# Performance work log

Measured on AMD Instinct MI355X. Metric: run time of the kernel, lower is better.

## Reference

```python
import jax, jax.numpy as jnp
import numpy as np

ALPHA = 16
M_FACTORS = [8, 16, 8]
N_FACTORS = [8, 16, 8]


def setup_inputs() -> dict:
    key = jax.random.key(0)
    ks = jax.random.split(key, 9)
    B, S, D = 8, 2048, 1024
    r = 8
    x = jax.random.normal(ks[0], (B, S, D), dtype=jnp.float32)
    W = jax.random.normal(ks[1], (D, D), dtype=jnp.float32) * 0.02
    b = jax.random.normal(ks[2], (D,), dtype=jnp.float32) * 0.02
    # m-cores: (r_prev, m_i, r_next), first rank = 1
    core0 = jax.random.normal(ks[3], (1, 8, r), dtype=jnp.float32) * 0.1
    core1 = jax.random.normal(ks[4], (r, 16, r), dtype=jnp.float32) * 0.1
    core2 = jax.random.normal(ks[5], (r, 8, r), dtype=jnp.float32) * 0.1
    # n-cores: (r_prev, n_i, r_next), last rank = 1
    core3 = jax.random.normal(ks[6], (r, 8, r), dtype=jnp.float32) * 0.1
    core4 = jax.random.normal(ks[7], (r, 16, r), dtype=jnp.float32) * 0.1
    core5 = jax.random.normal(ks[8], (r, 8, 1), dtype=jnp.float32) * 0.1
    return {"x": x, "W": W, "b": b, "core0": core0, "core1": core1,
            "core2": core2, "core3": core3, "core4": core4, "core5": core5}


def tensorized_multiplication(x, m_cores, n_cores, m_factors):
    B, S, _ = x.shape
    # [B, 1, S, m_k, ..., m_1] : input dim split into m_factors, reversed
    tt = x.reshape((B, S) + tuple(m_factors[::-1]))[:, None]
    for core in m_cores:
        # contract trailing m-factor and current rank, new rank at axis 1
        tt = jnp.einsum('br...m,rmp->bp...', tt, core)
    for core in n_cores:
        # expand n-factor at the end, carry rank at axis 1
        tt = jnp.einsum('br...,rnp->bp...n', tt, core)
    # tt: [B, 1, S, n_1, ..., n_k] -> [B, S, prod(n_factors)]
    return tt.reshape(B, S, -1)


def reference(x, W, b, core0, core1, core2, core3, core4, core5):
    z = tensorized_multiplication(x, [core0, core1, core2],
                                  [core3, core4, core5], M_FACTORS)
    base = jnp.einsum('bsd,od->bso', x, W) + b  # nn.Linear: x @ W.T + b
    return base + z * ALPHA
```

## Files before the change

### kernel.cpp

```cpp
#include <hip/hip_runtime.h>
#include <hip/hip_bf16.h>


#define D_DIM 1024
#define BS_ROWS 16384
#define ALPHA_F 16.0f
#define BM 128
#define BN 128

using bf16   = __bf16;
using bf16x8 = __attribute__((ext_vector_type(8))) __bf16;
using bf16x4 = __attribute__((ext_vector_type(4))) __bf16;
using f32x4  = __attribute__((ext_vector_type(4))) float;

#define GPTR(p) (const __attribute__((address_space(1))) void*)(p)
#define SPTR(p) (__attribute__((address_space(3))) void*)(p)

__global__ __launch_bounds__(256) void make_mn_kernel(
    const float* __restrict__ c0, const float* __restrict__ c1,
    const float* __restrict__ c2, const float* __restrict__ c3,
    const float* __restrict__ c4, const float* __restrict__ c5,
    float* __restrict__ Mws, float* __restrict__ NTws)
{
    __shared__ float sh[128 * 9];
    const int tid = threadIdx.x;

    if (blockIdx.x < 32) {
        for (int e = tid; e < 1024; e += 256) {
            int p2 = e & 7, i2i1 = e >> 3;
            int i1 = i2i1 & 7, i2 = i2i1 >> 3;
            float s = 0.f;
            for (int p1 = 0; p1 < 8; ++p1)
                s += c0[i1 * 8 + p1] * c1[p1 * 128 + i2 * 8 + p2];
            sh[i2i1 * 9 + p2] = s;
        }
        __syncthreads();
        int e = blockIdx.x * 256 + tid;
        int p3 = e & 7, d = e >> 3;
        int i1 = d & 7, i2 = (d >> 3) & 15, i3 = d >> 7;
        float s = 0.f;
        for (int p2 = 0; p2 < 8; ++p2)
            s += sh[(i2 * 8 + i1) * 9 + p2] * c2[p2 * 64 + i3 * 8 + p3];
        Mws[e] = s;
    } else {
        for (int e = tid; e < 1024; e += 256) {
            int p4 = e & 7, nn = e >> 3;
            int n2 = nn >> 3, n3 = nn & 7;
            float s = 0.f;
            for (int p5 = 0; p5 < 8; ++p5)
                s += c4[p4 * 128 + n2 * 8 + p5] * c5[p5 * 8 + n3];
            sh[nn * 9 + p4] = s;
        }
        __syncthreads();
        int e = (blockIdx.x - 32) * 256 + tid;
        int r3 = e & 7, o = e >> 3;
        int n1 = o >> 7, nn = o & 127;
        float s = 0.f;
        for (int p4 = 0; p4 < 8; ++p4)
            s += c3[r3 * 64 + n1 * 8 + p4] * sh[nn * 9 + p4];
        NTws[o * 8 + r3] = s;
    }
}

__global__ __launch_bounds__(256) void weff_cast_kernel(
    const float* __restrict__ X, const float* __restrict__ W,
    const float* __restrict__ Mws, const float* __restrict__ NTws,
    bf16* __restrict__ Weff, bf16* __restrict__ Xb)
{
    const int tid = threadIdx.x;
    if (blockIdx.x >= 512) {
        size_t i = ((size_t)(blockIdx.x - 512) * 256 + tid) * 8;
        f32x4 a = *(const f32x4*)&X[i];
        f32x4 b = *(const f32x4*)&X[i + 4];
        bf16x8 v;
        v[0] = (bf16)a[0]; v[1] = (bf16)a[1]; v[2] = (bf16)a[2]; v[3] = (bf16)a[3];
        v[4] = (bf16)b[0]; v[5] = (bf16)b[1]; v[6] = (bf16)b[2]; v[7] = (bf16)b[3];
        *(bf16x8*)&Xb[i] = v;
        return;
    }
    int e  = blockIdx.x * 256 + tid;
    int o  = e >> 7;
    int d0 = (e & 127) * 8;
    f32x4 nt0 = *(const f32x4*)&NTws[o * 8];
    f32x4 nt1 = *(const f32x4*)&NTws[o * 8 + 4];
    f32x4 w0 = *(const f32x4*)&W[(size_t)o * D_DIM + d0];
    f32x4 w1 = *(const f32x4*)&W[(size_t)o * D_DIM + d0 + 4];
    bf16x8 res;
    for (int k = 0; k < 8; ++k) {
        f32x4 m0 = *(const f32x4*)&Mws[(d0 + k) * 8];
        f32x4 m1 = *(const f32x4*)&Mws[(d0 + k) * 8 + 4];
        float acc = m0[0]*nt0[0] + m0[1]*nt0[1] + m0[2]*nt0[2] + m0[3]*nt0[3]
                  + m1[0]*nt1[0] + m1[1]*nt1[1] + m1[2]*nt1[2] + m1[3]*nt1[3];
        float w = (k < 4) ? w0[k] : w1[k - 4];
        res[k] = (bf16)(w + ALPHA_F * acc);
    }
    *(bf16x8*)&Weff[(size_t)o * D_DIM + d0] = res;
}

#define TBM 256
#define TBN 256
#define TBK 64
#define ABYT (TBM * TBK * 2)
#define BBYT (TBN * TBK * 2)
#define BUF5 (ABYT + BBYT)
#define NT5  (D_DIM / TBK)

__global__ __launch_bounds__(512, 2) void gemm_pipe5_kernel(
    const bf16* __restrict__ Xb,
    const bf16* __restrict__ Weff,
    const float* __restrict__ bias,
    float* __restrict__ Out)
{
    extern __shared__ __attribute__((aligned(16))) char smem[];

    const int tid  = threadIdx.x;
    const int wave = tid >> 6, lane = tid & 63;

    const int bid   = blockIdx.x;
    const int slot  = (bid & 7) * 32 + (bid >> 3);
    const int mtile = slot >> 2;
    const int ntile = slot & 3;

    const int wr = wave >> 2, wc = wave & 3;
    const int l15 = lane & 15, quad = lane >> 4;
    const int rsw = l15 & 7;

    const int srow   = wave * 32 + (lane >> 3);
    const int gchunk = (lane & 7) ^ (lane >> 3);
    const bf16* asrc = Xb   + (size_t)(mtile * TBM + srow) * D_DIM + gchunk * 8;
    const bf16* bsrc = Weff + (size_t)(ntile * TBN + srow) * D_DIM + gchunk * 8;
    const int woff = wave * 4096;

    auto STAGE = [&](int bo, int t) {
        const bf16* ap = asrc + t * TBK;
        const bf16* bp = bsrc + t * TBK;
#pragma unroll
        for (int j = 0; j < 4; ++j)
            __builtin_amdgcn_global_load_lds(GPTR(ap + (size_t)j * 8 * D_DIM),
                                             SPTR(smem + bo + woff + j * 1024), 16, 0, 0);
#pragma unroll
        for (int j = 0; j < 4; ++j)
            __builtin_amdgcn_global_load_lds(GPTR(bp + (size_t)j * 8 * D_DIM),
                                             SPTR(smem + bo + ABYT + woff + j * 1024), 16, 0, 0);
    };

    f32x4 acc[8][4];
#pragma unroll
    for (int i = 0; i < 8; ++i)
#pragma unroll
        for (int j = 0; j < 4; ++j)
#pragma unroll
            for (int r = 0; r < 4; ++r) acc[i][j][r] = 0.f;

    auto COMPUTE = [&](int bo) {
        const char* Ab = smem + bo;
        const char* Bb = smem + bo + ABYT;
#pragma unroll
        for (int kk = 0; kk < 2; ++kk) {
            const int sb = ((kk * 4 + quad) ^ rsw) * 16;
            bf16x8 bfr[4];
#pragma unroll
            for (int j = 0; j < 4; ++j)
                bfr[j] = *(const bf16x8*)(Bb + (wc * 64 + j * 16 + l15) * 128 + sb);
#pragma unroll
            for (int i = 0; i < 8; ++i) {
                bf16x8 af = *(const bf16x8*)(Ab + (wr * 128 + i * 16 + l15) * 128 + sb);
                __builtin_amdgcn_s_setprio(1);
#pragma unroll
                for (int j = 0; j < 4; ++j)
                    acc[i][j] = __builtin_amdgcn_mfma_f32_16x16x32_bf16(
                        af, bfr[j], acc[i][j], 0, 0, 0);
                __builtin_amdgcn_s_setprio(0);
            }
        }
    };

    STAGE(0, 0);
    asm volatile("s_waitcnt vmcnt(0)" ::: "memory");
    __builtin_amdgcn_s_barrier();
    __builtin_amdgcn_sched_barrier(0);

    int cur = 0;
    for (int t = 0; t < NT5 - 1; ++t) {
        STAGE((cur ^ 1) * BUF5, t + 1);
        COMPUTE(cur * BUF5);
        asm volatile("s_waitcnt vmcnt(0) lgkmcnt(0)" ::: "memory");
        __builtin_amdgcn_s_barrier();
        __builtin_amdgcn_sched_barrier(0);
        cur ^= 1;
    }
    COMPUTE(cur * BUF5);

    float bj[4];
#pragma unroll
    for (int j = 0; j < 4; ++j)
        bj[j] = bias[ntile * TBN + wc * 64 + j * 16 + l15];
#pragma unroll
    for (int i = 0; i < 8; ++i) {
        int row0 = mtile * TBM + wr * 128 + i * 16 + quad * 4;
#pragma unroll
        for (int r = 0; r < 4; ++r) {
            float* orow = Out + (size_t)(row0 + r) * D_DIM + ntile * TBN + wc * 64 + l15;
#pragma unroll
            for (int j = 0; j < 4; ++j)
                orow[j * 16] = acc[i][j][r] + bj[j];
        }
    }
}

__global__ __launch_bounds__(256) void gemm_bb_kernel(
    const bf16* __restrict__ Xb,
    const bf16* __restrict__ Weff,
    const float* __restrict__ bias,
    float* __restrict__ Out)
{
    __shared__ __align__(16) bf16 As[BM][64];
    __shared__ __align__(16) bf16 Bs[BN][64];

    const int tid  = threadIdx.x;
    const int wave = tid >> 6, lane = tid & 63;
    const int mtile = blockIdx.x, ntile = blockIdx.y;
    const int wr = wave >> 1, wc = wave & 1;
    const int l15 = lane & 15, quad = lane >> 4;

    const int srow = wave * 32 + (lane >> 3);
    const int gchunk = (lane & 7) ^ (lane >> 3);
    const bf16* asrc = Xb   + (size_t)(mtile * BM + srow) * D_DIM + gchunk * 8;
    const bf16* bsrc = Weff + (size_t)(ntile * BN + srow) * D_DIM + gchunk * 8;
    char* abase = (char*)&As[0][0] + wave * 4096;
    char* bbase = (char*)&Bs[0][0] + wave * 4096;

    const int rsw = l15 & 7;

    f32x4 acc[4][4];
    for (int i = 0; i < 4; ++i)
        for (int j = 0; j < 4; ++j)
            for (int r = 0; r < 4; ++r) acc[i][j][r] = 0.f;

    for (int kt = 0; kt < D_DIM / 64; ++kt) {
        const int ko = kt * 64;
        for (int j = 0; j < 4; ++j) {
            __builtin_amdgcn_global_load_lds(GPTR(asrc + (size_t)j * 8 * D_DIM + ko),
                                             SPTR(abase + j * 1024), 16, 0, 0);
            __builtin_amdgcn_global_load_lds(GPTR(bsrc + (size_t)j * 8 * D_DIM + ko),
                                             SPTR(bbase + j * 1024), 16, 0, 0);
        }
        __syncthreads();
        for (int kk = 0; kk < 2; ++kk) {
            const int lc = kk * 4 + quad;
            const int sc = (lc ^ rsw) * 8;
            bf16x8 af[4], bfr[4];
            for (int i = 0; i < 4; ++i)
                af[i] = *(const bf16x8*)&As[wr * 64 + i * 16 + l15][sc];
            for (int j = 0; j < 4; ++j)
                bfr[j] = *(const bf16x8*)&Bs[wc * 64 + j * 16 + l15][sc];
            for (int i = 0; i < 4; ++i)
                for (int j = 0; j < 4; ++j)
                    acc[i][j] = __builtin_amdgcn_mfma_f32_16x16x32_bf16(
                        af[i], bfr[j], acc[i][j], 0, 0, 0);
        }
        __syncthreads();
    }

    float bj[4];
    for (int j = 0; j < 4; ++j)
        bj[j] = bias[ntile * BN + wc * 64 + j * 16 + l15];
    for (int i = 0; i < 4; ++i) {
        int row0 = mtile * BM + wr * 64 + i * 16 + quad * 4;
        for (int r = 0; r < 4; ++r) {
            float* orow = Out + (size_t)(row0 + r) * D_DIM + ntile * BN + wc * 64 + l15;
            for (int j = 0; j < 4; ++j)
                orow[j * 16] = acc[i][j][r] + bj[j];
        }
    }
}

__global__ __launch_bounds__(256) void gemm_bias_kernel(
    const float* __restrict__ X,
    const bf16* __restrict__ Weff,
    const float* __restrict__ bias,
    float* __restrict__ Out)
{
    __shared__ __align__(16) bf16 As[BM][32];
    __shared__ __align__(16) bf16 Bs[BN][32];

    const int tid  = threadIdx.x;
    const int wave = tid >> 6, lane = tid & 63;
    const int mtile = blockIdx.x, ntile = blockIdx.y;
    const int wr = wave >> 1, wc = wave & 1;
    const int l15 = lane & 15, quad = lane >> 4;

    const int ar = tid >> 1, ah = tid & 1;
    const float* xsrc = X + (size_t)(mtile * BM + ar) * D_DIM + ah * 16;
    bf16* adst = &As[ar][ah * 16];

    const bf16* bsrc0 = Weff + (size_t)(ntile * BN + wave * 32 + (lane >> 2)) * D_DIM
                        + (lane & 3) * 8;
    const bf16* bsrc1 = bsrc0 + 16 * D_DIM;
    char* bbase = (char*)&Bs[0][0];
    void* bdst0 = bbase + wave * 2048;
    void* bdst1 = bbase + wave * 2048 + 1024;

    f32x4 acc[4][4];
    for (int i = 0; i < 4; ++i)
        for (int j = 0; j < 4; ++j)
            for (int r = 0; r < 4; ++r) acc[i][j][r] = 0.f;

    for (int kt = 0; kt < D_DIM / 32; ++kt) {
        __builtin_amdgcn_global_load_lds(GPTR(bsrc0 + kt * 32), SPTR(bdst0), 16, 0, 0);
        __builtin_amdgcn_global_load_lds(GPTR(bsrc1 + kt * 32), SPTR(bdst1), 16, 0, 0);

        const f32x4* xp = (const f32x4*)(xsrc + kt * 32);
        f32x4 f0 = xp[0], f1 = xp[1], f2 = xp[2], f3 = xp[3];
        bf16x8 p0, p1;
        p0[0] = (bf16)f0[0]; p0[1] = (bf16)f0[1]; p0[2] = (bf16)f0[2]; p0[3] = (bf16)f0[3];
        p0[4] = (bf16)f1[0]; p0[5] = (bf16)f1[1]; p0[6] = (bf16)f1[2]; p0[7] = (bf16)f1[3];
        p1[0] = (bf16)f2[0]; p1[1] = (bf16)f2[1]; p1[2] = (bf16)f2[2]; p1[3] = (bf16)f2[3];
        p1[4] = (bf16)f3[0]; p1[5] = (bf16)f3[1]; p1[6] = (bf16)f3[2]; p1[7] = (bf16)f3[3];
        *(bf16x8*)adst = p0;
        *(bf16x8*)(adst + 8) = p1;

        __syncthreads();

        bf16x8 af[4], bfr[4];
        for (int i = 0; i < 4; ++i)
            af[i] = *(const bf16x8*)&As[wr * 64 + i * 16 + l15][quad * 8];
        for (int j = 0; j < 4; ++j)
            bfr[j] = *(const bf16x8*)&Bs[wc * 64 + j * 16 + l15][quad * 8];
        for (int i = 0; i < 4; ++i)
            for (int j = 0; j < 4; ++j)
                acc[i][j] = __builtin_amdgcn_mfma_f32_16x16x32_bf16(
                    af[i], bfr[j], acc[i][j], 0, 0, 0);

        __syncthreads();
    }

    float bj[4];
    for (int j = 0; j < 4; ++j)
        bj[j] = bias[ntile * BN + wc * 64 + j * 16 + l15];
    for (int i = 0; i < 4; ++i) {
        int row0 = mtile * BM + wr * 64 + i * 16 + quad * 4;
        for (int r = 0; r < 4; ++r) {
            float* orow = Out + (size_t)(row0 + r) * D_DIM + ntile * BN + wc * 64 + l15;
            for (int j = 0; j < 4; ++j)
                orow[j * 16] = acc[i][j][r] + bj[j];
        }
    }
}

__global__ __launch_bounds__(256) void build_weff_fused_kernel(
    const float* __restrict__ W,
    const float* __restrict__ c0, const float* __restrict__ c1,
    const float* __restrict__ c2, const float* __restrict__ c3,
    const float* __restrict__ c4, const float* __restrict__ c5,
    bf16* __restrict__ Weff)
{
    __shared__ float t2[1024];
    __shared__ float Msh[8192];
    const int tid = threadIdx.x;
    const int o = blockIdx.x;

    for (int e = tid; e < 1024; e += 256) {
        int p2 = e & 7, i2i1 = e >> 3;
        int i1 = i2i1 & 7, i2 = i2i1 >> 3;
        float s = 0.f;
        for (int p1 = 0; p1 < 8; ++p1)
            s += c0[i1 * 8 + p1] * c1[p1 * 128 + i2 * 8 + p2];
        t2[e] = s;
    }
    __syncthreads();
    for (int e = tid; e < 8192; e += 256) {
        int p3 = e & 7, d = e >> 3;
        int i1 = d & 7, i2 = (d >> 3) & 15, i3 = d >> 7;
        float s = 0.f;
        for (int p2 = 0; p2 < 8; ++p2)
            s += t2[(i2 * 8 + i1) * 8 + p2] * c2[p2 * 64 + i3 * 8 + p3];
        Msh[e] = s;
    }
    int n1 = o >> 7, nn = o & 127, n2 = nn >> 3, n3 = nn & 7;
    float v[8];
    for (int p4 = 0; p4 < 8; ++p4) {
        float s = 0.f;
        for (int p5 = 0; p5 < 8; ++p5)
            s += c4[p4 * 128 + n2 * 8 + p5] * c5[p5 * 8 + n3];
        v[p4] = s;
    }
    float ncol[8];
    for (int r3 = 0; r3 < 8; ++r3) {
        float s = 0.f;
        for (int p4 = 0; p4 < 8; ++p4)
            s += c3[r3 * 64 + n1 * 8 + p4] * v[p4];
        ncol[r3] = s;
    }
    __syncthreads();

    int d0 = tid * 4;
    f32x4 w = *(const f32x4*)&W[o * D_DIM + d0];
    bf16x4 res;
    for (int k = 0; k < 4; ++k) {
        float acc = 0.f;
        for (int r = 0; r < 8; ++r)
            acc += Msh[(d0 + k) * 8 + r] * ncol[r];
        res[k] = (bf16)(w[k] + ALPHA_F * acc);
    }
    *(bf16x4*)&Weff[o * D_DIM + d0] = res;
}

extern "C" void kernel_launch(void* const* d_in, const int* in_sizes, int n_in,
                              void* d_out, int out_size, void* d_ws, size_t ws_size,
                              hipStream_t stream) {
    const float* x  = (const float*)d_in[0];
    const float* W  = (const float*)d_in[1];
    const float* b  = (const float*)d_in[2];
    const float* c0 = (const float*)d_in[3];
    const float* c1 = (const float*)d_in[4];
    const float* c2 = (const float*)d_in[5];
    const float* c3 = (const float*)d_in[6];
    const float* c4 = (const float*)d_in[7];
    const float* c5 = (const float*)d_in[8];
    float* out = (float*)d_out;

    char* ws = (char*)d_ws;
    bf16*  Weff = (bf16*)ws;
    float* Mws  = (float*)(ws + 2u * 1024u * 1024u);
    float* NTws = Mws + 8192;
    bf16*  Xb   = (bf16*)(ws + 4u * 1024u * 1024u);
    const size_t need = 4u * 1024u * 1024u + (size_t)BS_ROWS * D_DIM * 2u;

    static int smem_ok = -1;
    if (smem_ok < 0) {
        hipError_t e = hipFuncSetAttribute((const void*)gemm_pipe5_kernel,
                                           hipFuncAttributeMaxDynamicSharedMemorySize,
                                           2 * BUF5);
        smem_ok = (e == hipSuccess) ? 1 : 0;
    }

    if (ws_size >= need) {
        make_mn_kernel<<<64, 256, 0, stream>>>(c0, c1, c2, c3, c4, c5, Mws, NTws);
        weff_cast_kernel<<<512 + 8192, 256, 0, stream>>>(x, W, Mws, NTws, Weff, Xb);
        if (smem_ok) {
            gemm_pipe5_kernel<<<dim3(256), 512, 2 * BUF5, stream>>>(Xb, Weff, b, out);
        } else {
            dim3 grid(BS_ROWS / BM, D_DIM / BN);
            gemm_bb_kernel<<<grid, 256, 0, stream>>>(Xb, Weff, b, out);
        }
    } else {
        build_weff_fused_kernel<<<D_DIM, 256, 0, stream>>>(W, c0, c1, c2, c3, c4, c5, Weff);
        dim3 grid(BS_ROWS / BM, D_DIM / BN);
        gemm_bias_kernel<<<grid, 256, 0, stream>>>(x, Weff, b, out);
    }
}
```

Measured before the change: 164.9 us.

## Interleave next-tile loads with MFMA phases in a ping-pong GEMM schedule

Rewrites the GEMM main loop so each K-step runs in four phases. The global-to-LDS loads for the next tile are issued in units between the early phases, and LDS reads of A fragments are split per phase, with barriers that keep waves in lockstep. The aim is to overlap memory traffic with MFMA work more finely and reduce LDS-read stalls ahead of the matrix ops. The extra barriers per phase add synchronisation overhead, and the staging layout changes to 128-row units.

```diff
diff --git a/kernel.cpp b/kernel.cpp
--- a/kernel.cpp
+++ b/kernel.cpp
@@ -100,12 +100,11 @@
 #define TBM 256
 #define TBN 256
 #define TBK 64
-#define ABYT (TBM * TBK * 2)
-#define BBYT (TBN * TBK * 2)
-#define BUF5 (ABYT + BBYT)
-#define NT5  (D_DIM / TBK)
-
-__global__ __launch_bounds__(512, 2) void gemm_pipe5_kernel(
+#define ABYT 32768
+#define BUF6 65536
+#define NT6  (D_DIM / TBK)
+
+__global__ __launch_bounds__(512, 2) void gemm_pipe6_kernel(
     const bf16* __restrict__ Xb,
     const bf16* __restrict__ Weff,
     const float* __restrict__ bias,
@@ -125,71 +124,89 @@
     const int l15 = lane & 15, quad = lane >> 4;
     const int rsw = l15 & 7;
 
-    const int srow   = wave * 32 + (lane >> 3);
+    const int urow   = wave * 8 + (lane >> 3);
     const int gchunk = (lane & 7) ^ (lane >> 3);
-    const bf16* asrc = Xb   + (size_t)(mtile * TBM + srow) * D_DIM + gchunk * 8;
-    const bf16* bsrc = Weff + (size_t)(ntile * TBN + srow) * D_DIM + gchunk * 8;
-    const int woff = wave * 4096;
-
-    auto STAGE = [&](int bo, int t) {
-        const bf16* ap = asrc + t * TBK;
-        const bf16* bp = bsrc + t * TBK;
+    const bf16* aB = Xb   + (size_t)(mtile * TBM) * D_DIM + gchunk * 8;
+    const bf16* bB = Weff + (size_t)(ntile * TBN) * D_DIM + gchunk * 8;
+    const int lco = wave * 1024 + lane * 16;
+
+    auto STAGE_UNIT = [&](int bo, int t, int u) {
+        const bf16* src = (u < 2)
+            ? aB + (size_t)(u * 128 + urow) * D_DIM + t * TBK
+            : bB + (size_t)((u - 2) * 128 + urow) * D_DIM + t * TBK;
+        char* dst = smem + bo + (u < 2 ? 0 : ABYT) + (u & 1) * 16384 + lco;
+#pragma unroll
+        for (int j = 0; j < 2; ++j)
+            __builtin_amdgcn_global_load_lds(GPTR(src + (size_t)j * 64 * D_DIM),
+                                             SPTR(dst + j * 8192), 16, 0, 0);
+    };
+
+    f32x4 acc[8][4];
+#pragma unroll
+    for (int i = 0; i < 8; ++i)
 #pragma unroll
         for (int j = 0; j < 4; ++j)
-            __builtin_amdgcn_global_load_lds(GPTR(ap + (size_t)j * 8 * D_DIM),
-                                             SPTR(smem + bo + woff + j * 1024), 16, 0, 0);
-#pragma unroll
-        for (int j = 0; j < 4; ++j)
-            __builtin_amdgcn_global_load_lds(GPTR(bp + (size_t)j * 8 * D_DIM),
-                                             SPTR(smem + bo + ABYT + woff + j * 1024), 16, 0, 0);
-    };
-
-    f32x4 acc[8][4];
-#pragma unroll
-    for (int i = 0; i < 8; ++i)
-#pragma unroll
-        for (int j = 0; j < 4; ++j)
 #pragma unroll
             for (int r = 0; r < 4; ++r) acc[i][j][r] = 0.f;
 
-    auto COMPUTE = [&](int bo) {
-        const char* Ab = smem + bo;
-        const char* Bb = smem + bo + ABYT;
-#pragma unroll
-        for (int kk = 0; kk < 2; ++kk) {
-            const int sb = ((kk * 4 + quad) ^ rsw) * 16;
-            bf16x8 bfr[4];
-#pragma unroll
-            for (int j = 0; j < 4; ++j)
-                bfr[j] = *(const bf16x8*)(Bb + (wc * 64 + j * 16 + l15) * 128 + sb);
-#pragma unroll
-            for (int i = 0; i < 8; ++i) {
-                bf16x8 af = *(const bf16x8*)(Ab + (wr * 128 + i * 16 + l15) * 128 + sb);
-                __builtin_amdgcn_s_setprio(1);
-#pragma unroll
-                for (int j = 0; j < 4; ++j)
-                    acc[i][j] = __builtin_amdgcn_mfma_f32_16x16x32_bf16(
-                        af, bfr[j], acc[i][j], 0, 0, 0);
-                __builtin_amdgcn_s_setprio(0);
-            }
-        }
-    };
-
-    STAGE(0, 0);
+    STAGE_UNIT(0, 0, 2); STAGE_UNIT(0, 0, 3);
+    STAGE_UNIT(0, 0, 0); STAGE_UNIT(0, 0, 1);
     asm volatile("s_waitcnt vmcnt(0)" ::: "memory");
     __builtin_amdgcn_s_barrier();
     __builtin_amdgcn_sched_barrier(0);
 
-    int cur = 0;
-    for (int t = 0; t < NT5 - 1; ++t) {
-        STAGE((cur ^ 1) * BUF5, t + 1);
-        COMPUTE(cur * BUF5);
-        asm volatile("s_waitcnt vmcnt(0) lgkmcnt(0)" ::: "memory");
-        __builtin_amdgcn_s_barrier();
-        __builtin_amdgcn_sched_barrier(0);
-        cur ^= 1;
-    }
-    COMPUTE(cur * BUF5);
+    for (int t = 0; t < NT6; ++t) {
+        const int bo = (t & 1) * BUF6;
+        const int bn = ((t + 1) & 1) * BUF6;
+        const bool more = (t + 1 < NT6);
+        const char* Ab = smem + bo;
+        const char* Bb = smem + bo + ABYT;
+
+        bf16x8 bfr[4][2];
+#pragma unroll
+        for (int p = 0; p < 4; ++p) {
+            if (p == 0 && more) { STAGE_UNIT(bn, t + 1, 2); STAGE_UNIT(bn, t + 1, 3); }
+            if (p == 1 && more) { STAGE_UNIT(bn, t + 1, 0); STAGE_UNIT(bn, t + 1, 1); }
+
+            if (p == 0) {
+#pragma unroll
+                for (int j = 0; j < 4; ++j)
+#pragma unroll
+                    for (int kk = 0; kk < 2; ++kk)
+                        bfr[j][kk] = *(const bf16x8*)(Bb
+                            + (wc * 64 + j * 16 + l15) * 128
+                            + ((kk * 4 + quad) ^ rsw) * 16);
+            }
+            bf16x8 af[2][2];
+#pragma unroll
+            for (int ii = 0; ii < 2; ++ii)
+#pragma unroll
+                for (int kk = 0; kk < 2; ++kk)
+                    af[ii][kk] = *(const bf16x8*)(Ab
+                        + (wr * 128 + (2 * p + ii) * 16 + l15) * 128
+                        + ((kk * 4 + quad) ^ rsw) * 16);
+
+            __builtin_amdgcn_s_barrier();
+            asm volatile("s_waitcnt lgkmcnt(0)" ::: "memory");
+            __builtin_amdgcn_s_setprio(1);
+#pragma unroll
+            for (int kk = 0; kk < 2; ++kk)
+#pragma unroll
+                for (int ii = 0; ii < 2; ++ii)
+#pragma unroll
+                    for (int j = 0; j < 4; ++j)
+                        acc[2 * p + ii][j] = __builtin_amdgcn_mfma_f32_16x16x32_bf16(
+                            af[ii][kk], bfr[j][kk], acc[2 * p + ii][j], 0, 0, 0);
+            __builtin_amdgcn_s_setprio(0);
+            if (p < 3) __builtin_amdgcn_s_barrier();
+        }
+
+        if (more) {
+            asm volatile("s_waitcnt vmcnt(0)" ::: "memory");
+            __builtin_amdgcn_s_barrier();
+            __builtin_amdgcn_sched_barrier(0);
+        }
+    }
 
     float bj[4];
 #pragma unroll
@@ -429,9 +446,9 @@
 
     static int smem_ok = -1;
     if (smem_ok < 0) {
-        hipError_t e = hipFuncSetAttribute((const void*)gemm_pipe5_kernel,
+        hipError_t e = hipFuncSetAttribute((const void*)gemm_pipe6_kernel,
                                            hipFuncAttributeMaxDynamicSharedMemorySize,
-                                           2 * BUF5);
+                                           2 * BUF6);
         smem_ok = (e == hipSuccess) ? 1 : 0;
     }
 
@@ -439,7 +456,7 @@
         make_mn_kernel<<<64, 256, 0, stream>>>(c0, c1, c2, c3, c4, c5, Mws, NTws);
         weff_cast_kernel<<<512 + 8192, 256, 0, stream>>>(x, W, Mws, NTws, Weff, Xb);
         if (smem_ok) {
-            gemm_pipe5_kernel<<<dim3(256), 512, 2 * BUF5, stream>>>(Xb, Weff, b, out);
+            gemm_pipe6_kernel<<<dim3(256), 512, 2 * BUF6, stream>>>(Xb, Weff, b, out);
         } else {
             dim3 grid(BS_ROWS / BM, D_DIM / BN);
             gemm_bb_kernel<<<grid, 256, 0, stream>>>(Xb, Weff, b, out);
```

Measured after the change: 165.5 us. No clear change (+0.4%).
